# Optimization experiments

Measured on AMD Instinct MI355X. Metric: run time of the kernel, lower is better.

Reference implementation:

```python
import jax, jax.numpy as jnp
import numpy as np

D_MODEL = 1024
N_HEADS = 16
HEAD_DIM = D_MODEL // N_HEADS
D_FF = 4096
RANK = 8
B, T = 4, 2048


def _layernorm(x, g, b, eps=1e-5):
    mu = jnp.mean(x, axis=-1, keepdims=True)
    var = jnp.var(x, axis=-1, keepdims=True)
    return (x - mu) * jax.lax.rsqrt(var + eps) * g + b


def _dyn_linear(x, W, A, b_dyn, bias=None):
    # base: x [b,t,i] @ W.T  (W is [o,i] like nn.Linear)
    out = jnp.einsum('bti,oi->bto', x, W)
    if bias is not None:
        out = out + bias
    # per-sample low-rank delta: (x @ b_dyn.T) @ A.T
    delta = jnp.einsum('bti,bri,or->bto', x, b_dyn, A)
    return out + delta


def setup_inputs() -> dict:
    key = jax.random.key(0)
    ks = jax.random.split(key, 24)
    s = 0.02
    inp = {
        'x': jax.random.normal(ks[0], (B, T, D_MODEL), jnp.float32),
        'dyn_q': jax.random.normal(ks[1], (B, RANK, D_MODEL), jnp.float32) * s,
        'dyn_k': jax.random.normal(ks[2], (B, RANK, D_MODEL), jnp.float32) * s,
        'dyn_v': jax.random.normal(ks[3], (B, RANK, D_MODEL), jnp.float32) * s,
        'dyn_ff1': jax.random.normal(ks[4], (B, RANK, D_MODEL), jnp.float32) * s,
        'dyn_ff2': jax.random.normal(ks[5], (B, RANK, D_FF), jnp.float32) * s,
        'Wq': jax.random.normal(ks[6], (D_MODEL, D_MODEL), jnp.float32) / np.sqrt(D_MODEL),
        'Aq': jax.random.normal(ks[7], (D_MODEL, RANK), jnp.float32) * s,
        'Wk': jax.random.normal(ks[8], (D_MODEL, D_MODEL), jnp.float32) / np.sqrt(D_MODEL),
        'Ak': jax.random.normal(ks[9], (D_MODEL, RANK), jnp.float32) * s,
        'Wv': jax.random.normal(ks[10], (D_MODEL, D_MODEL), jnp.float32) / np.sqrt(D_MODEL),
        'Av': jax.random.normal(ks[11], (D_MODEL, RANK), jnp.float32) * s,
        'Wo': jax.random.normal(ks[12], (D_MODEL, D_MODEL), jnp.float32) / np.sqrt(D_MODEL),
        'W1': jax.random.normal(ks[13], (D_FF, D_MODEL), jnp.float32) / np.sqrt(D_MODEL),
        'b1': jnp.zeros((D_FF,), jnp.float32),
        'A1': jax.random.normal(ks[14], (D_FF, RANK), jnp.float32) * s,
        'W2': jax.random.normal(ks[15], (D_MODEL, D_FF), jnp.float32) / np.sqrt(D_FF),
        'b2': jnp.zeros((D_MODEL,), jnp.float32),
        'A2': jax.random.normal(ks[16], (D_MODEL, RANK), jnp.float32) * s,
        'g1': jnp.ones((D_MODEL,), jnp.float32),
        'beta1': jnp.zeros((D_MODEL,), jnp.float32),
        'g2': jnp.ones((D_MODEL,), jnp.float32),
        'beta2': jnp.zeros((D_MODEL,), jnp.float32),
    }
    return inp


def reference(x, dyn_q, dyn_k, dyn_v, dyn_ff1, dyn_ff2,
              Wq, Aq, Wk, Ak, Wv, Av, Wo,
              W1, b1, A1, W2, b2, A2,
              g1, beta1, g2, beta2):
    bsz, seq_len, _ = x.shape
    residual = x
    h = _layernorm(x, g1, beta1)
    q = _dyn_linear(h, Wq, Aq, dyn_q)
    k = _dyn_linear(h, Wk, Ak, dyn_k)
    v = _dyn_linear(h, Wv, Av, dyn_v)
    # [b, t, h, d] -> [b, h, t, d]
    q = q.reshape(bsz, seq_len, N_HEADS, HEAD_DIM).transpose(0, 2, 1, 3)
    k = k.reshape(bsz, seq_len, N_HEADS, HEAD_DIM).transpose(0, 2, 1, 3)
    v = v.reshape(bsz, seq_len, N_HEADS, HEAD_DIM).transpose(0, 2, 1, 3)
    score = jnp.einsum('bhqd,bhkd->bhqk', q, k) / np.sqrt(HEAD_DIM).astype(np.float32)
    attn = jax.nn.softmax(score, axis=-1)
    ctx = jnp.einsum('bhqk,bhkd->bhqd', attn, v)
    ctx = ctx.transpose(0, 2, 1, 3).reshape(bsz, seq_len, D_MODEL)
    x = residual + jnp.einsum('bti,oi->bto', ctx, Wo)  # dropout p=0
    residual = x
    h = _layernorm(x, g2, beta2)
    ff = jax.nn.gelu(_dyn_linear(h, W1, A1, dyn_ff1, bias=b1), approximate=False)
    ff = _dyn_linear(ff, W2, A2, dyn_ff2, bias=b2)
    return residual + ff
```

## Files before the change

### kernel.cpp

```cpp
#include <hip/hip_runtime.h>
#include <math.h>

#define D_MODEL 1024
#define D_FF    4096
#define RANK    8
#define BATCH   4
#define SEQ     2048
#define MTOT    (BATCH*SEQ)
#define NHEADS  16
#define HDIM    64

typedef __attribute__((ext_vector_type(8))) __bf16 bf16x8;
typedef __attribute__((ext_vector_type(4))) float f32x4;
typedef __attribute__((ext_vector_type(8))) unsigned short u16x8;
typedef __attribute__((ext_vector_type(4))) unsigned short u16x4;

__device__ __forceinline__ unsigned short f2bf(float f) {
  __bf16 h = (__bf16)f;
  return __builtin_bit_cast(unsigned short, h);
}
__device__ __forceinline__ float bf2f(unsigned short h) {
  union { unsigned int u; float f; } v; v.u = ((unsigned int)h) << 16;
  return v.f;
}

__device__ __forceinline__ f32x4 mfma16(bf16x8 a, bf16x8 b, f32x4 c) {
  return __builtin_amdgcn_mfma_f32_16x16x32_bf16(a, b, c, 0, 0, 0);
}

#define GLDS(g, l) __builtin_amdgcn_global_load_lds( \
    (const __attribute__((address_space(1))) void*)(g), \
    (__attribute__((address_space(3))) void*)(l), 16, 0, 0)

__global__ __launch_bounds__(256) void cvt_bf16(const float* __restrict__ in,
                                                unsigned short* __restrict__ out, int n8)
{
  int i = blockIdx.x * 256 + threadIdx.x;
  if (i >= n8) return;
  const float4 a  = *reinterpret_cast<const float4*>(in + (size_t)i * 8);
  const float4 b  = *reinterpret_cast<const float4*>(in + (size_t)i * 8 + 4);
  u16x8 o;
  o[0] = f2bf(a.x); o[1] = f2bf(a.y); o[2] = f2bf(a.z); o[3] = f2bf(a.w);
  o[4] = f2bf(b.x); o[5] = f2bf(b.y); o[6] = f2bf(b.z); o[7] = f2bf(b.w);
  *reinterpret_cast<u16x8*>(out + (size_t)i * 8) = o;
}

__global__ __launch_bounds__(256) void ln_fwd(const float* __restrict__ x,
                                              const float* __restrict__ g,
                                              const float* __restrict__ be,
                                              unsigned short* __restrict__ out)
{
  const int row = blockIdx.x;
  const int t = threadIdx.x;
  const float* xr = x + (size_t)row * D_MODEL;
  float4 vv = *reinterpret_cast<const float4*>(xr + t * 4);
  float s  = vv.x + vv.y + vv.z + vv.w;
  float s2 = vv.x * vv.x + vv.y * vv.y + vv.z * vv.z + vv.w * vv.w;
#pragma unroll
  for (int mm = 1; mm < 64; mm <<= 1) { s += __shfl_xor(s, mm); s2 += __shfl_xor(s2, mm); }
  __shared__ float red[8];
  const int w = t >> 6, l = t & 63;
  if (l == 0) { red[w] = s; red[4 + w] = s2; }
  __syncthreads();
  s  = red[0] + red[1] + red[2] + red[3];
  s2 = red[4] + red[5] + red[6] + red[7];
  float mean = s * (1.f / D_MODEL);
  float var  = s2 * (1.f / D_MODEL) - mean * mean;
  float rstd = rsqrtf(var + 1e-5f);
  float4 gv = *reinterpret_cast<const float4*>(g  + t * 4);
  float4 bv = *reinterpret_cast<const float4*>(be + t * 4);
  u16x4 o;
  o[0] = f2bf((vv.x - mean) * rstd * gv.x + bv.x);
  o[1] = f2bf((vv.y - mean) * rstd * gv.y + bv.y);
  o[2] = f2bf((vv.z - mean) * rstd * gv.z + bv.z);
  o[3] = f2bf((vv.w - mean) * rstd * gv.w + bv.w);
  *reinterpret_cast<u16x4*>(out + (size_t)row * D_MODEL + t * 4) = o;
}

template<int ILEN>
__global__ __launch_bounds__(256) void dyn_u(const unsigned short* __restrict__ hmat,
                                             const float* __restrict__ dyn,
                                             float* __restrict__ u)
{
  const int tid = threadIdx.x, w = tid >> 6, l = tid & 63;
  const int m0 = blockIdx.x * 16 + w * 4;
  const int b = m0 / SEQ;
  const float* dynb = dyn + (size_t)b * RANK * ILEN;
  float acc[4][RANK] = {};
  for (int s = 0; s < ILEN / 64; ++s) {
    const int i = l + s * 64;
    float hv[4];
#pragma unroll
    for (int rr = 0; rr < 4; ++rr) hv[rr] = bf2f(hmat[(size_t)(m0 + rr) * ILEN + i]);
#pragma unroll
    for (int r = 0; r < RANK; ++r) {
      float d = dynb[(size_t)r * ILEN + i];
#pragma unroll
      for (int rr = 0; rr < 4; ++rr) acc[rr][r] += hv[rr] * d;
    }
  }
#pragma unroll
  for (int rr = 0; rr < 4; ++rr)
#pragma unroll
    for (int r = 0; r < RANK; ++r) {
      float a = acc[rr][r];
#pragma unroll
      for (int mm = 1; mm < 64; mm <<= 1) a += __shfl_xor(a, mm);
      if (l == 0) u[(size_t)(m0 + rr) * RANK + r] = a;
    }
}

__global__ __launch_bounds__(256) void dyn_u_qkv(const unsigned short* __restrict__ hmat,
                                                 const float* __restrict__ dq,
                                                 const float* __restrict__ dk,
                                                 const float* __restrict__ dv,
                                                 float* __restrict__ u)
{
  const int tid = threadIdx.x, w = tid >> 6, l = tid & 63;
  const int m0 = blockIdx.x * 16 + w * 4;
  const int b = m0 / SEQ;
  const float* db0 = dq + (size_t)b * RANK * D_MODEL;
  const float* db1 = dk + (size_t)b * RANK * D_MODEL;
  const float* db2 = dv + (size_t)b * RANK * D_MODEL;
  float acc[4][3 * RANK] = {};
  for (int s = 0; s < D_MODEL / 64; ++s) {
    const int i = l + s * 64;
    float hv[4];
#pragma unroll
    for (int rr = 0; rr < 4; ++rr) hv[rr] = bf2f(hmat[(size_t)(m0 + rr) * D_MODEL + i]);
#pragma unroll
    for (int r = 0; r < RANK; ++r) {
      float d0 = db0[(size_t)r * D_MODEL + i];
      float d1 = db1[(size_t)r * D_MODEL + i];
      float d2 = db2[(size_t)r * D_MODEL + i];
#pragma unroll
      for (int rr = 0; rr < 4; ++rr) {
        acc[rr][r] += hv[rr] * d0;
        acc[rr][RANK + r] += hv[rr] * d1;
        acc[rr][2 * RANK + r] += hv[rr] * d2;
      }
    }
  }
#pragma unroll
  for (int g = 0; g < 3; ++g)
#pragma unroll
    for (int rr = 0; rr < 4; ++rr)
#pragma unroll
      for (int r = 0; r < RANK; ++r) {
        float a = acc[rr][g * RANK + r];
#pragma unroll
        for (int mm = 1; mm < 64; mm <<= 1) a += __shfl_xor(a, mm);
        if (l == 0) u[((size_t)g * MTOT + m0 + rr) * RANK + r] = a;
      }
}

template<int NDIM, int KDIM, int MODE>
__global__ __launch_bounds__(512, 2) void gemm_bt(const unsigned short* __restrict__ A,
                                                  const unsigned short* __restrict__ B,
                                                  void* __restrict__ outp,
                                                  void* __restrict__ outp2,
                                                  const float* __restrict__ uvec,
                                                  const float* __restrict__ Ad0,
                                                  const float* __restrict__ Ad1,
                                                  const float* __restrict__ Ad2,
                                                  const float* __restrict__ bias,
                                                  const float* __restrict__ resid)
{
  constexpr bool HAS_DYN = (MODE == 2 || MODE == 3 || MODE == 5);
  __shared__ unsigned short sAB[2][(256 + 128) * 64];
  const int tid = threadIdx.x;
  const int w = tid >> 6, l = tid & 63;

  constexpr int NBX = NDIM / 128;
  constexpr int NWG = NBX * (MTOT / 256);
  const int bid = blockIdx.y * NBX + blockIdx.x;
  const int sbid = (bid & 7) * (NWG / 8) + (bid >> 3);
  const int tm = (sbid / NBX) * 256, tn = (sbid % NBX) * 128;
  const int wm = w >> 1, wn = w & 1;

  f32x4 acc[4][4] = {};

  const int srow = l >> 3;
  const int sc8 = (l & 7) ^ (srow & 7);
  const unsigned short* Ag = A + (size_t)(tm + srow) * KDIM + sc8 * 8;
  const unsigned short* Bg = B + (size_t)(tn + srow) * KDIM + sc8 * 8;

  const int arow = wm * 64 + (l & 15);
  const int bcol = wn * 64 + (l & 15);
  const int kb0 = l >> 4;
  const int swz = l & 7;

  constexpr int NT = KDIM / 64;

  auto stage = [&](int buf, int kt) {
    unsigned short* bA = &sAB[buf][0];
    unsigned short* bB = &sAB[buf][256 * 64];
#pragma unroll
    for (int it = 0; it < 4; ++it) {
      const int st = w * 4 + it;
      GLDS(Ag + (size_t)(st * 8) * KDIM + kt, bA + st * 512);
    }
#pragma unroll
    for (int it = 0; it < 2; ++it) {
      const int st = w * 2 + it;
      GLDS(Bg + (size_t)(st * 8) * KDIM + kt, bB + st * 512);
    }
  };

  stage(0, 0);
  asm volatile("s_waitcnt vmcnt(0)" ::: "memory");
  __syncthreads();

  int cur = 0;
  for (int t = 0; t < NT; ++t) {
    if (t + 1 < NT) stage(cur ^ 1, (t + 1) * 64);

    const unsigned short* sA_ = &sAB[cur][0];
    const unsigned short* sB_ = &sAB[cur][256 * 64];
#pragma unroll
    for (int kk = 0; kk < 2; ++kk) {
      bf16x8 af[4], bfv[4];
      const int kphys = ((kk * 4 + kb0) ^ swz) << 3;
#pragma unroll
      for (int i = 0; i < 4; ++i)
        af[i] = *reinterpret_cast<const bf16x8*>(&sA_[(arow + i * 16) * 64 + kphys]);
#pragma unroll
      for (int j = 0; j < 4; ++j)
        bfv[j] = *reinterpret_cast<const bf16x8*>(&sB_[(bcol + j * 16) * 64 + kphys]);
#pragma unroll
      for (int i = 0; i < 4; ++i)
#pragma unroll
        for (int j = 0; j < 4; ++j)
          acc[i][j] = mfma16(af[i], bfv[j], acc[i][j]);
    }
    __syncthreads();
    cur ^= 1;
  }

  const int rbase = tm + wm * 64 + ((l >> 4) << 2);
  const int cbase = tn + wn * 64 + (l & 15);

  const int seg = tn >> 10;
  const float* Ad = Ad0;
  const float* uv = uvec;
  if constexpr (MODE == 5) {
    Ad = (seg == 0) ? Ad0 : (seg == 1) ? Ad1 : Ad2;
    uv = uvec + (size_t)seg * ((size_t)MTOT * RANK);
  }

#pragma unroll
  for (int i = 0; i < 4; ++i) {
    float uu[4][8];
    if constexpr (HAS_DYN) {
#pragma unroll
      for (int r = 0; r < 4; ++r) {
        const float* up = uv + (size_t)(rbase + i * 16 + r) * RANK;
#pragma unroll
        for (int p = 0; p < 8; ++p) uu[r][p] = up[p];
      }
    }
#pragma unroll
    for (int j = 0; j < 4; ++j) {
      const int col = cbase + j * 16;
      float ad[8];
      if constexpr (HAS_DYN) {
#pragma unroll
        for (int p = 0; p < 8; ++p) ad[p] = Ad[(size_t)col * RANK + p];
      }
      float vv4[4];
#pragma unroll
      for (int r = 0; r < 4; ++r) {
        const int row = rbase + i * 16 + r;
        float v = acc[i][j][r];
        if constexpr (HAS_DYN) {
#pragma unroll
          for (int p = 0; p < 8; ++p) v += uu[r][p] * ad[p];
        }
        if constexpr (MODE == 2) {
          v += bias[col];
          v = 0.5f * v * (1.f + erff(v * 0.70710678118654752f));
        }
        if constexpr (MODE == 1) {
          v += resid[(size_t)row * NDIM + col];
        }
        if constexpr (MODE == 3) {
          v += bias[col] + resid[(size_t)row * NDIM + col];
        }
        if constexpr (MODE == 5) {
          if (seg == 0) v *= 0.18033688011112042f;
        }
        vv4[r] = v;
      }
      if constexpr (MODE == 2) {
#pragma unroll
        for (int r = 0; r < 4; ++r)
          ((unsigned short*)outp)[(size_t)(rbase + i * 16 + r) * NDIM + col] = f2bf(vv4[r]);
      } else if constexpr (MODE == 5) {
        const int cl = col & 1023;
        if (seg < 2) {
#pragma unroll
          for (int r = 0; r < 4; ++r)
            ((unsigned short*)outp)[((size_t)seg * MTOT + rbase + i * 16 + r) * D_MODEL + cl] =
                f2bf(vv4[r]);
        } else {
          const int row0 = rbase + i * 16;
          const int bb = row0 >> 11, tt = row0 & (SEQ - 1);
          const int hh = cl >> 6, dd = cl & 63;
          u16x4 o;
          o[0] = f2bf(vv4[0]); o[1] = f2bf(vv4[1]); o[2] = f2bf(vv4[2]); o[3] = f2bf(vv4[3]);
          *reinterpret_cast<u16x4*>(
              &((unsigned short*)outp2)[(((size_t)bb * NHEADS + hh) * HDIM + dd) * SEQ + tt]) = o;
        }
      } else {
#pragma unroll
        for (int r = 0; r < 4; ++r)
          ((float*)outp)[(size_t)(rbase + i * 16 + r) * NDIM + col] = vv4[r];
      }
    }
  }
}

__global__ __launch_bounds__(256, 4) void attn_fwd(const unsigned short* __restrict__ q,
                                                   const unsigned short* __restrict__ k,
                                                   const unsigned short* __restrict__ vt,
                                                   unsigned short* __restrict__ ctx)
{
  __shared__ unsigned short sK[128 * 64];
  __shared__ unsigned short sV[64 * 128];
  __shared__ unsigned short sP[4][32 * 64];

  const int tid = threadIdx.x, w = tid >> 6, l = tid & 63;
  const int lin = blockIdx.y * (SEQ / 128) + blockIdx.x;
  const int W = (lin & 7) * ((BATCH * NHEADS * SEQ / 128) / 8) + (lin >> 3);
  const int bh = W >> 4, b = bh >> 4, hh = bh & 15;
  const int q0 = (W & 15) * 128 + w * 32;
  const size_t base = ((size_t)b * SEQ) * D_MODEL + hh * HDIM;
  const size_t vtbase = (size_t)bh * HDIM * SEQ;

  bf16x8 qf[2][2];
#pragma unroll
  for (int i = 0; i < 2; ++i)
#pragma unroll
    for (int ks = 0; ks < 2; ++ks)
      qf[i][ks] = *reinterpret_cast<const bf16x8*>(
          &q[base + (size_t)(q0 + i * 16 + (l & 15)) * D_MODEL + ks * 32 + (l >> 4) * 8]);

  float mrun[2][4], lrun[2][4];
  f32x4 oacc[2][4] = {};
#pragma unroll
  for (int i = 0; i < 2; ++i)
#pragma unroll
    for (int r = 0; r < 4; ++r) { mrun[i][r] = -3.0e38f; lrun[i][r] = 0.f; }

  const int krow_l = l >> 3;
  const int kswz = (l & 7) ^ (krow_l & 7);
  const unsigned short* kg = k + base + (size_t)krow_l * D_MODEL + kswz * 8;
  const int vrow_l = l >> 4;
  const int vswz = (l & 15) ^ (((w & 1) * 4 + vrow_l) & 7);
  const unsigned short* vg = vt + vtbase + (size_t)vrow_l * SEQ + vswz * 8;

  const int swz = l & 7;
  const int kb0 = l >> 4;

  for (int kt = 0; kt < SEQ; kt += 128) {
    __syncthreads();
#pragma unroll
    for (int it = 0; it < 4; ++it) {
      const int r4 = it * 4 + w;
      GLDS(kg + (size_t)(kt + r4 * 8) * D_MODEL, sK + r4 * 512);
      GLDS(vg + (size_t)(r4 * 4) * SEQ + kt, sV + r4 * 512);
    }
    asm volatile("s_waitcnt vmcnt(0)" ::: "memory");
    __syncthreads();

    f32x4 sacc[2][8] = {};
    __builtin_amdgcn_s_setprio(1);
#pragma unroll
    for (int ks = 0; ks < 2; ++ks) {
#pragma unroll
      for (int j = 0; j < 8; ++j) {
        const int row = j * 16 + (l & 15);
        bf16x8 kf = *reinterpret_cast<const bf16x8*>(
            &sK[row * 64 + (((ks * 4 + kb0) ^ swz) << 3)]);
#pragma unroll
        for (int i = 0; i < 2; ++i) sacc[i][j] = mfma16(qf[i][ks], kf, sacc[i][j]);
      }
    }
    __builtin_amdgcn_s_setprio(0);

    float pr[2][4][4];
#pragma unroll
    for (int i = 0; i < 2; ++i) {
#pragma unroll
      for (int r = 0; r < 4; ++r) {
        float sv[8];
#pragma unroll
        for (int j = 0; j < 8; ++j) sv[j] = sacc[i][j][r];
        float mx = fmaxf(fmaxf(fmaxf(sv[0], sv[1]), fmaxf(sv[2], sv[3])),
                         fmaxf(fmaxf(sv[4], sv[5]), fmaxf(sv[6], sv[7])));
#pragma unroll
        for (int mm = 1; mm < 16; mm <<= 1) mx = fmaxf(mx, __shfl_xor(mx, mm, 16));
        const float mnew = fmaxf(mrun[i][r], mx);
        const float alpha = __builtin_exp2f(mrun[i][r] - mnew);
        mrun[i][r] = mnew;
        float p[8], ps = 0.f;
#pragma unroll
        for (int j = 0; j < 8; ++j) { p[j] = __builtin_exp2f(sv[j] - mnew); ps += p[j]; }
#pragma unroll
        for (int mm = 1; mm < 16; mm <<= 1) ps += __shfl_xor(ps, mm, 16);
        lrun[i][r] = lrun[i][r] * alpha + ps;
        const int prow = i * 16 + ((l >> 4) << 2) + r;
        const int pswz = prow & 7;
        unsigned short* pb = &sP[w][prow * 64];
        const int chi = (l & 15) >> 3, clo = l & 7;
        pb[(((0 + chi) ^ pswz) << 3) + clo] = f2bf(p[0]);
        pb[(((2 + chi) ^ pswz) << 3) + clo] = f2bf(p[1]);
        pb[(((4 + chi) ^ pswz) << 3) + clo] = f2bf(p[2]);
        pb[(((6 + chi) ^ pswz) << 3) + clo] = f2bf(p[3]);
#pragma unroll
        for (int jj = 0; jj < 4; ++jj) pr[i][r][jj] = p[4 + jj];
#pragma unroll
        for (int j = 0; j < 4; ++j) oacc[i][j][r] *= alpha;
      }
    }

    __builtin_amdgcn_s_setprio(1);
#pragma unroll
    for (int ks = 0; ks < 2; ++ks) {
      bf16x8 pf[2];
#pragma unroll
      for (int i = 0; i < 2; ++i) {
        const int prw = i * 16 + (l & 15);
        pf[i] = *reinterpret_cast<const bf16x8*>(
            &sP[w][prw * 64 + (((ks * 4 + kb0) ^ (prw & 7)) << 3)]);
      }
#pragma unroll
      for (int j = 0; j < 4; ++j) {
        const int row = j * 16 + (l & 15);
        bf16x8 vf = *reinterpret_cast<const bf16x8*>(
            &sV[row * 128 + (((ks * 4 + kb0) ^ swz) << 3)]);
#pragma unroll
        for (int i = 0; i < 2; ++i) oacc[i][j] = mfma16(pf[i], vf, oacc[i][j]);
      }
    }
    __builtin_amdgcn_s_setprio(0);

#pragma unroll
    for (int i = 0; i < 2; ++i) {
#pragma unroll
      for (int r = 0; r < 4; ++r) {
        const int prow = i * 16 + ((l >> 4) << 2) + r;
        const int pswz = prow & 7;
        unsigned short* pb = &sP[w][prow * 64];
        const int chi = (l & 15) >> 3, clo = l & 7;
        pb[(((0 + chi) ^ pswz) << 3) + clo] = f2bf(pr[i][r][0]);
        pb[(((2 + chi) ^ pswz) << 3) + clo] = f2bf(pr[i][r][1]);
        pb[(((4 + chi) ^ pswz) << 3) + clo] = f2bf(pr[i][r][2]);
        pb[(((6 + chi) ^ pswz) << 3) + clo] = f2bf(pr[i][r][3]);
      }
    }

    __builtin_amdgcn_s_setprio(1);
#pragma unroll
    for (int ks = 0; ks < 2; ++ks) {
      bf16x8 pf[2];
#pragma unroll
      for (int i = 0; i < 2; ++i) {
        const int prw = i * 16 + (l & 15);
        pf[i] = *reinterpret_cast<const bf16x8*>(
            &sP[w][prw * 64 + (((ks * 4 + kb0) ^ (prw & 7)) << 3)]);
      }
#pragma unroll
      for (int j = 0; j < 4; ++j) {
        const int row = j * 16 + (l & 15);
        bf16x8 vf = *reinterpret_cast<const bf16x8*>(
            &sV[row * 128 + (((8 + ks * 4 + kb0) ^ swz) << 3)]);
#pragma unroll
        for (int i = 0; i < 2; ++i) oacc[i][j] = mfma16(pf[i], vf, oacc[i][j]);
      }
    }
    __builtin_amdgcn_s_setprio(0);
  }

#pragma unroll
  for (int i = 0; i < 2; ++i)
#pragma unroll
    for (int r = 0; r < 4; ++r) {
      float inv = 1.f / lrun[i][r];
      int row = q0 + i * 16 + ((l >> 4) << 2) + r;
#pragma unroll
      for (int j = 0; j < 4; ++j)
        ctx[base + (size_t)row * D_MODEL + j * 16 + (l & 15)] = f2bf(oacc[i][j][r] * inv);
    }
}

extern "C" void kernel_launch(void* const* d_in, const int* in_sizes, int n_in,
                              void* d_out, int out_size, void* d_ws, size_t ws_size,
                              hipStream_t stream)
{
  (void)in_sizes; (void)n_in; (void)out_size; (void)ws_size;
  const float* x      = (const float*)d_in[0];
  const float* dyn_q  = (const float*)d_in[1];
  const float* dyn_k  = (const float*)d_in[2];
  const float* dyn_v  = (const float*)d_in[3];
  const float* dyn_f1 = (const float*)d_in[4];
  const float* dyn_f2 = (const float*)d_in[5];
  const float* Wq = (const float*)d_in[6];
  const float* Aq = (const float*)d_in[7];
  const float* Wk = (const float*)d_in[8];
  const float* Ak = (const float*)d_in[9];
  const float* Wv = (const float*)d_in[10];
  const float* Av = (const float*)d_in[11];
  const float* Wo = (const float*)d_in[12];
  const float* W1 = (const float*)d_in[13];
  const float* b1 = (const float*)d_in[14];
  const float* A1 = (const float*)d_in[15];
  const float* W2 = (const float*)d_in[16];
  const float* b2 = (const float*)d_in[17];
  const float* A2 = (const float*)d_in[18];
  const float* g1 = (const float*)d_in[19];
  const float* be1 = (const float*)d_in[20];
  const float* g2 = (const float*)d_in[21];
  const float* be2 = (const float*)d_in[22];

  char* ws = (char*)d_ws;
  size_t o = 0;
  auto take = [&](size_t b) { size_t r = o; o += (b + 255) & ~(size_t)255; return r; };
  const size_t o_wq = take((size_t)D_MODEL * D_MODEL * 2);
  const size_t o_wk = take((size_t)D_MODEL * D_MODEL * 2);
  const size_t o_wv = take((size_t)D_MODEL * D_MODEL * 2);
  const size_t o_wo = take((size_t)D_MODEL * D_MODEL * 2);
  const size_t o_w1 = take((size_t)D_FF * D_MODEL * 2);
  const size_t o_w2 = take((size_t)D_FF * D_MODEL * 2);
  const size_t o_h1 = take((size_t)MTOT * D_MODEL * 2);
  const size_t o_q  = take((size_t)MTOT * D_MODEL * 2);
  const size_t o_k  = take((size_t)MTOT * D_MODEL * 2);
  const size_t o_v  = take((size_t)MTOT * D_MODEL * 2);
  const size_t o_u  = take((size_t)MTOT * RANK * 4 * 3);
  const size_t o_ff = take((size_t)MTOT * D_FF * 2);

  unsigned short* wq_b = (unsigned short*)(ws + o_wq);
  unsigned short* wk_b = (unsigned short*)(ws + o_wk);
  unsigned short* wv_b = (unsigned short*)(ws + o_wv);
  unsigned short* wo_b = (unsigned short*)(ws + o_wo);
  unsigned short* w1_b = (unsigned short*)(ws + o_w1);
  unsigned short* w2_b = (unsigned short*)(ws + o_w2);
  unsigned short* h1   = (unsigned short*)(ws + o_h1);
  unsigned short* qb   = (unsigned short*)(ws + o_q);
  unsigned short* vtb  = (unsigned short*)(ws + o_v);
  float* u_q  = (float*)(ws + o_u);
  float* u_k  = u_q + (size_t)MTOT * RANK;
  unsigned short* ctx = h1;
  float* x2 = (float*)(ws + o_q);
  unsigned short* h2 = vtb;
  float* u_f1 = u_q;
  float* u_f2 = u_k;
  unsigned short* ffb = (unsigned short*)(ws + o_ff);

  cvt_bf16<<<512,  256, 0, stream>>>(Wq, wq_b, (D_MODEL * D_MODEL) / 8);
  cvt_bf16<<<512,  256, 0, stream>>>(Wk, wk_b, (D_MODEL * D_MODEL) / 8);
  cvt_bf16<<<512,  256, 0, stream>>>(Wv, wv_b, (D_MODEL * D_MODEL) / 8);
  cvt_bf16<<<512,  256, 0, stream>>>(Wo, wo_b, (D_MODEL * D_MODEL) / 8);
  cvt_bf16<<<2048, 256, 0, stream>>>(W1, w1_b, (D_FF * D_MODEL) / 8);
  cvt_bf16<<<2048, 256, 0, stream>>>(W2, w2_b, (D_FF * D_MODEL) / 8);

  ln_fwd<<<MTOT, 256, 0, stream>>>(x, g1, be1, h1);

  dyn_u_qkv<<<MTOT / 16, 256, 0, stream>>>(h1, dyn_q, dyn_k, dyn_v, u_q);

  gemm_bt<3 * D_MODEL, D_MODEL, 5><<<dim3(3 * D_MODEL / 128, MTOT / 256), 512, 0, stream>>>(
      h1, wq_b, qb, vtb, u_q, Aq, Ak, Av, nullptr, nullptr);

  attn_fwd<<<dim3(SEQ / 128, BATCH * NHEADS), 256, 0, stream>>>(
      qb, qb + (size_t)MTOT * D_MODEL, vtb, ctx);

  gemm_bt<D_MODEL, D_MODEL, 1><<<dim3(D_MODEL / 128, MTOT / 256), 512, 0, stream>>>(
      ctx, wo_b, x2, nullptr, nullptr, nullptr, nullptr, nullptr, nullptr, x);

  ln_fwd<<<MTOT, 256, 0, stream>>>(x2, g2, be2, h2);

  dyn_u<D_MODEL><<<MTOT / 16, 256, 0, stream>>>(h2, dyn_f1, u_f1);
  gemm_bt<D_FF, D_MODEL, 2><<<dim3(D_FF / 128, MTOT / 256), 512, 0, stream>>>(
      h2, w1_b, ffb, nullptr, u_f1, A1, nullptr, nullptr, b1, nullptr);

  dyn_u<D_FF><<<MTOT / 16, 256, 0, stream>>>(ffb, dyn_f2, u_f2);
  gemm_bt<D_MODEL, D_FF, 3><<<dim3(D_MODEL / 128, MTOT / 256), 512, 0, stream>>>(
      ffb, w2_b, (float*)d_out, nullptr, u_f2, A2, nullptr, nullptr, b2, x2);
}
```

Before: 623.4 us.

## Permute key order in V^T layout and P tile to enable packed LDS stores

The V^T output of the QKV projection is now written in a permuted token order within each 64-token block. This lets each lane in the attention kernel write its four softmax probabilities as a single 8-byte LDS store instead of four scalar 2-byte stores. The P and V layouts must stay consistent for P·V to remain correct, because both are permuted the same way. The cost is scattered scalar global stores in the V^T epilogue, which replace the earlier 8-byte vector store.

```diff
diff --git a/kernel.cpp b/kernel.cpp
--- a/kernel.cpp
+++ b/kernel.cpp
@@ -304,12 +304,14 @@
                 f2bf(vv4[r]);
         } else {
           const int row0 = rbase + i * 16;
-          const int bb = row0 >> 11, tt = row0 & (SEQ - 1);
+          const int bb = row0 >> 11, t0 = row0 & (SEQ - 1);
           const int hh = cl >> 6, dd = cl & 63;
-          u16x4 o;
-          o[0] = f2bf(vv4[0]); o[1] = f2bf(vv4[1]); o[2] = f2bf(vv4[2]); o[3] = f2bf(vv4[3]);
-          *reinterpret_cast<u16x4*>(
-              &((unsigned short*)outp2)[(((size_t)bb * NHEADS + hh) * HDIM + dd) * SEQ + tt]) = o;
+          const int jj = (t0 >> 4) & 3;
+          unsigned short* vb = &((unsigned short*)outp2)[
+              (((size_t)bb * NHEADS + hh) * HDIM + dd) * SEQ + (t0 & ~63)];
+#pragma unroll
+          for (int dlt = 0; dlt < 4; ++dlt)
+            vb[((t0 & 15) + dlt) * 4 + jj] = f2bf(vv4[dlt]);
         }
       } else {
 #pragma unroll
@@ -389,6 +391,7 @@
     __builtin_amdgcn_s_setprio(0);
 
     float pr[2][4][4];
+    const int c15 = l & 15;
 #pragma unroll
     for (int i = 0; i < 2; ++i) {
 #pragma unroll
@@ -410,13 +413,10 @@
         for (int mm = 1; mm < 16; mm <<= 1) ps += __shfl_xor(ps, mm, 16);
         lrun[i][r] = lrun[i][r] * alpha + ps;
         const int prow = i * 16 + ((l >> 4) << 2) + r;
-        const int pswz = prow & 7;
-        unsigned short* pb = &sP[w][prow * 64];
-        const int chi = (l & 15) >> 3, clo = l & 7;
-        pb[(((0 + chi) ^ pswz) << 3) + clo] = f2bf(p[0]);
-        pb[(((2 + chi) ^ pswz) << 3) + clo] = f2bf(p[1]);
-        pb[(((4 + chi) ^ pswz) << 3) + clo] = f2bf(p[2]);
-        pb[(((6 + chi) ^ pswz) << 3) + clo] = f2bf(p[3]);
+        u16x4 pk;
+        pk[0] = f2bf(p[0]); pk[1] = f2bf(p[1]); pk[2] = f2bf(p[2]); pk[3] = f2bf(p[3]);
+        *reinterpret_cast<u16x4*>(
+            &sP[w][prow * 64 + ((((c15 >> 1) ^ (prow & 7)) << 3) | ((c15 & 1) << 2))]) = pk;
 #pragma unroll
         for (int jj = 0; jj < 4; ++jj) pr[i][r][jj] = p[4 + jj];
 #pragma unroll
@@ -450,13 +450,11 @@
 #pragma unroll
       for (int r = 0; r < 4; ++r) {
         const int prow = i * 16 + ((l >> 4) << 2) + r;
-        const int pswz = prow & 7;
-        unsigned short* pb = &sP[w][prow * 64];
-        const int chi = (l & 15) >> 3, clo = l & 7;
-        pb[(((0 + chi) ^ pswz) << 3) + clo] = f2bf(pr[i][r][0]);
-        pb[(((2 + chi) ^ pswz) << 3) + clo] = f2bf(pr[i][r][1]);
-        pb[(((4 + chi) ^ pswz) << 3) + clo] = f2bf(pr[i][r][2]);
-        pb[(((6 + chi) ^ pswz) << 3) + clo] = f2bf(pr[i][r][3]);
+        u16x4 pk;
+        pk[0] = f2bf(pr[i][r][0]); pk[1] = f2bf(pr[i][r][1]);
+        pk[2] = f2bf(pr[i][r][2]); pk[3] = f2bf(pr[i][r][3]);
+        *reinterpret_cast<u16x4*>(
+            &sP[w][prow * 64 + ((((c15 >> 1) ^ (prow & 7)) << 3) | ((c15 & 1) << 2))]) = pk;
       }
     }
 
```

Result: no change. 621.3 us (-0.3%).
